# Performance work log

Measured on AMD Instinct MI355X. Metric: run time of the kernel, lower is better.

Reference implementation:

```python
import jax, jax.numpy as jnp
import numpy as np

N, E, B = 50000, 800000, 64
D_IN, D_E = 192, 64
NUM_OUT = 256


def setup_inputs() -> dict:
    key = jax.random.key(0)
    ks = jax.random.split(key, 30)
    rn = lambda k, s: jax.random.normal(k, s, dtype=jnp.float32) * 0.05
    return {
        "x": jax.random.normal(ks[0], (N, D_IN), jnp.float32),
        "edge_index": jax.random.randint(ks[1], (2, E), 0, N, dtype=jnp.int32),
        "edge_attr": jax.random.normal(ks[2], (E, D_E), jnp.float32),
        "batch": jnp.sort(jax.random.randint(ks[3], (N,), 0, B, dtype=jnp.int32)),
        "W1": rn(ks[4], (D_IN, 256)), "as1": rn(ks[5], (4, 64)), "ad1": rn(ks[6], (4, 64)),
        "We1": rn(ks[7], (D_E, 256)), "ae1": rn(ks[8], (4, 64)), "b1": rn(ks[9], (256,)),
        "W2": rn(ks[10], (256, 256)), "as2": rn(ks[11], (4, 64)), "ad2": rn(ks[12], (4, 64)),
        "We2": rn(ks[13], (D_E, 256)), "ae2": rn(ks[14], (4, 64)), "b2": rn(ks[15], (256,)),
        "W3": rn(ks[16], (256, 512)), "as3": rn(ks[17], (4, 128)), "ad3": rn(ks[18], (4, 128)),
        "We3": rn(ks[19], (D_E, 512)), "ae3": rn(ks[20], (4, 128)), "b3": rn(ks[21], (128,)),
        "Wa": rn(ks[22], (128, NUM_OUT)), "ba": rn(ks[23], (NUM_OUT,)),
        "Wv": rn(ks[24], (128, 1)), "bv": rn(ks[25], (1,)),
    }


def reference(x, edge_index, edge_attr, batch,
              W1, as1, ad1, We1, ae1, b1,
              W2, as2, ad2, We2, ae2, b2,
              W3, as3, ad3, We3, ae3, b3,
              Wa, ba, Wv, bv):
    Nn = x.shape[0]
    src0, dst0 = edge_index[0], edge_index[1]
    # PyG add_self_loops(fill_value='mean'): self-loop edge_attr = mean of incoming edge_attr
    deg = jax.ops.segment_sum(jnp.ones_like(dst0, dtype=x.dtype), dst0, num_segments=Nn)
    loop_attr = jax.ops.segment_sum(edge_attr, dst0, num_segments=Nn) / jnp.maximum(deg, 1.0)[:, None]
    loop = jnp.arange(Nn, dtype=src0.dtype)
    src = jnp.concatenate([src0, loop])
    dst = jnp.concatenate([dst0, loop])
    ea = jnp.concatenate([edge_attr, loop_attr], axis=0)

    def gat(h, W, a_s, a_d, We, a_e, bias, concat):
        Hh, C = a_s.shape
        hs = (h @ W).reshape(Nn, Hh, C)                       # [N,H,C]
        al_s = (hs * a_s).sum(-1)                             # [N,H]
        al_d = (hs * a_d).sum(-1)                             # [N,H]
        al_e = ((ea @ We).reshape(-1, Hh, C) * a_e).sum(-1)   # [E+N,H]
        alpha = jax.nn.leaky_relu(al_s[src] + al_d[dst] + al_e, 0.2)
        amax = jax.ops.segment_max(alpha, dst, num_segments=Nn)
        w = jnp.exp(alpha - amax[dst])
        denom = jax.ops.segment_sum(w, dst, num_segments=Nn)
        w = w / (denom[dst] + 1e-16)                          # scatter-softmax over dst
        out = jax.ops.segment_sum(hs[src] * w[..., None], dst, num_segments=Nn)
        out = out.reshape(Nn, Hh * C) if concat else out.mean(axis=1)
        return out + bias

    h = jax.nn.relu(gat(x, W1, as1, ad1, We1, ae1, b1, True))
    h = jax.nn.relu(gat(h, W2, as2, ad2, We2, ae2, b2, True))
    h = gat(h, W3, as3, ad3, We3, ae3, b3, False)
    cnt = jax.ops.segment_sum(jnp.ones((Nn,), h.dtype), batch, num_segments=B)
    g = jax.ops.segment_sum(h, batch, num_segments=B) / jnp.maximum(cnt, 1.0)[:, None]
    logits = g @ Wa + ba
    value = g @ Wv + bv
    return jnp.concatenate([logits, value], axis=-1)  # [B, num_outputs+1]
```

## Files before the change

### kernel.cpp

```cpp
#include <hip/hip_runtime.h>
#include <hip/hip_bf16.h>


typedef __attribute__((ext_vector_type(8))) short short8;
typedef __attribute__((ext_vector_type(4))) float floatx4;

#define DEV __device__ __forceinline__

DEV unsigned short f2b(float f) {
  union { float f; unsigned u; } v; v.f = f;
  unsigned r = v.u + 0x7FFFu + ((v.u >> 16) & 1u);
  return (unsigned short)(r >> 16);
}
DEV float b2f(unsigned short u) {
  union { unsigned u; float f; } v; v.u = ((unsigned)u) << 16;
  return v.f;
}

__global__ void k_deg(const int* __restrict__ dst, int* __restrict__ deg, int E) {
  int e = blockIdx.x * 256 + threadIdx.x;
  if (e < E) atomicAdd(&deg[dst[e]], 1);
}

__global__ __launch_bounds__(256) void k_scan1(const int* __restrict__ deg,
    int* __restrict__ rowptr, int* __restrict__ bsum, int N) {
  __shared__ int sd[256];
  int b = blockIdx.x, tid = threadIdx.x;
  int i0 = b * 1024 + tid * 4;
  int v[4]; int s = 0;
#pragma unroll
  for (int j = 0; j < 4; j++) { int i = i0 + j; v[j] = (i < N) ? deg[i] : 0; s += v[j]; }
  sd[tid] = s;
  __syncthreads();
  for (int off = 1; off < 256; off <<= 1) {
    int t = (tid >= off) ? sd[tid - off] : 0;
    __syncthreads();
    sd[tid] += t;
    __syncthreads();
  }
  int run = sd[tid] - s;
#pragma unroll
  for (int j = 0; j < 4; j++) { int i = i0 + j; if (i < N) rowptr[i] = run; run += v[j]; }
  if (tid == 255) bsum[b] = sd[255];
}

__global__ __launch_bounds__(256) void k_scan2(int* __restrict__ bsum, int nb) {
  __shared__ int sd[256];
  int tid = threadIdx.x;
  int v = (tid < nb) ? bsum[tid] : 0;
  sd[tid] = v;
  __syncthreads();
  for (int off = 1; off < 256; off <<= 1) {
    int t = (tid >= off) ? sd[tid - off] : 0;
    __syncthreads();
    sd[tid] += t;
    __syncthreads();
  }
  if (tid < nb) bsum[tid] = sd[tid] - v;
}

__global__ __launch_bounds__(256) void k_scan3(int* __restrict__ rowptr,
    int* __restrict__ cursor, const int* __restrict__ bsum, int N, int E) {
  int b = blockIdx.x, tid = threadIdx.x;
  int add = bsum[b];
  int i0 = b * 1024 + tid * 4;
#pragma unroll
  for (int j = 0; j < 4; j++) {
    int i = i0 + j;
    if (i < N) { int r = rowptr[i] + add; rowptr[i] = r; cursor[i] = r; }
  }
  if (b == 0 && tid == 0) rowptr[N] = E;
}

__global__ void k_scatter(const int* __restrict__ src, const int* __restrict__ dst,
    int* __restrict__ cursor, int2* __restrict__ csr, int E) {
  int e = blockIdx.x * 256 + threadIdx.x;
  if (e < E) {
    int d = dst[e];
    int pos = atomicAdd(&cursor[d], 1);
    csr[pos] = make_int2(src[e], e);
  }
}

__global__ void k_wt(const float* __restrict__ W, unsigned short* __restrict__ Wt,
                     int K, int Nout) {
  int idx = blockIdx.x * 256 + threadIdx.x;
  if (idx < K * Nout) {
    int n = idx / K, k = idx - n * K;
    Wt[idx] = f2b(W[(size_t)k * Nout + n]);
  }
}

__global__ void k_wep(const float* __restrict__ We1, const float* __restrict__ ae1,
                      const float* __restrict__ We2, const float* __restrict__ ae2,
                      const float* __restrict__ We3, const float* __restrict__ ae3,
                      unsigned short* __restrict__ Wept) {
  int t = blockIdx.x * 256 + threadIdx.x;
  int j = t >> 6, c = t & 63;
  int L = j >> 2, h = j & 3;
  const float* We = (L == 0) ? We1 : (L == 1) ? We2 : We3;
  const float* ae = (L == 0) ? ae1 : (L == 1) ? ae2 : ae3;
  int C = (L == 2) ? 128 : 64;
  int HC = 4 * C;
  float s = 0.f;
  for (int cc = 0; cc < C; cc++) s += We[(size_t)c * HC + h * C + cc] * ae[h * C + cc];
  Wept[j * 64 + c] = f2b(s);
  if (t < 256) {
    int jj = 12 + (t >> 6);
    Wept[jj * 64 + (t & 63)] = 0;
  }
}

template<bool A_F32, int OUT_MODE, bool DO_ALD>
__global__ __launch_bounds__(256) void k_gemm(const void* __restrict__ Ap,
    const unsigned short* __restrict__ Bt, void* __restrict__ Cp,
    int M, int Nout, int K, int EN,
    const float* __restrict__ a_s, const float* __restrict__ a_d,
    float* __restrict__ als, float* __restrict__ ald) {
  __shared__ unsigned short As[64][40];
  __shared__ unsigned short Bs[64][40];
  const int tid = threadIdx.x;
  const int wave = tid >> 6, lane = tid & 63;
  const int quad = lane >> 4, l16 = lane & 15;
  const int m0 = blockIdx.x * 64, n0 = blockIdx.y * 64;
  const int arow = tid >> 2, acg = (tid & 3) * 8;
  floatx4 acc[4] = {{0,0,0,0},{0,0,0,0},{0,0,0,0},{0,0,0,0}};
  for (int k0 = 0; k0 < K; k0 += 32) {
    {
      int gm = m0 + arow;
      unsigned short tmp[8];
      if (A_F32) {
        const float* Af = (const float*)Ap;
        if (gm < M) {
          const float4* p = (const float4*)(Af + (size_t)gm * K + k0 + acg);
          float4 u0 = p[0], u1 = p[1];
          tmp[0]=f2b(u0.x); tmp[1]=f2b(u0.y); tmp[2]=f2b(u0.z); tmp[3]=f2b(u0.w);
          tmp[4]=f2b(u1.x); tmp[5]=f2b(u1.y); tmp[6]=f2b(u1.z); tmp[7]=f2b(u1.w);
        } else {
#pragma unroll
          for (int j = 0; j < 8; j++) tmp[j] = 0;
        }
      } else {
        const unsigned short* Ab = (const unsigned short*)Ap;
        uint4 u = {0,0,0,0};
        if (gm < M) u = *(const uint4*)(Ab + (size_t)gm * K + k0 + acg);
        *(uint4*)tmp = u;
      }
      *(uint4*)&As[arow][acg] = *(uint4*)tmp;
      int gn = n0 + arow;
      uint4 bv = {0,0,0,0};
      if (gn < Nout) bv = *(const uint4*)(Bt + (size_t)gn * K + k0 + acg);
      *(uint4*)&Bs[arow][acg] = bv;
    }
    __syncthreads();
    short8 a = *(const short8*)&As[wave * 16 + l16][quad * 8];
#pragma unroll
    for (int t = 0; t < 4; t++) {
      short8 b = *(const short8*)&Bs[t * 16 + l16][quad * 8];
      acc[t] = __builtin_amdgcn_mfma_f32_16x16x32_bf16(a, b, acc[t], 0, 0, 0);
    }
    __syncthreads();
  }
#pragma unroll
  for (int t = 0; t < 4; t++) {
#pragma unroll
    for (int r = 0; r < 4; r++) {
      int row = m0 + wave * 16 + quad * 4 + r;
      int col = n0 + t * 16 + l16;
      float v = acc[t][r];
      if (OUT_MODE == 0) {
        if (row < M && col < Nout)
          ((unsigned short*)Cp)[(size_t)row * Nout + col] = f2b(v);
      } else {
        if (row < M && col < 12)
          ((float*)Cp)[((size_t)(col >> 2) * EN + row) * 4 + (col & 3)] = v;
      }
    }
  }
  if constexpr (DO_ALD) {
    int h = (n0 * 4) / Nout;
#pragma unroll
    for (int r = 0; r < 4; r++) {
      float ps = 0.f, pd = 0.f;
#pragma unroll
      for (int t = 0; t < 4; t++) {
        int col = n0 + t * 16 + l16;
        float v = acc[t][r];
        ps += v * a_s[col];
        pd += v * a_d[col];
      }
#pragma unroll
      for (int off = 1; off < 16; off <<= 1) {
        ps += __shfl_xor(ps, off, 64);
        pd += __shfl_xor(pd, off, 64);
      }
      int row = m0 + wave * 16 + quad * 4 + r;
      if (l16 == 0 && row < M) {
        atomicAdd(&als[row * 4 + h], ps);
        atomicAdd(&ald[row * 4 + h], pd);
      }
    }
  }
}

__global__ void k_loop_ale(const int* __restrict__ rowptr, const int2* __restrict__ csr,
                           float* __restrict__ ale, int N, int E) {
  int n = blockIdx.x * 256 + threadIdx.x;
  if (n >= N) return;
  const size_t EN = (size_t)E + N;
  int s = rowptr[n], e = rowptr[n + 1];
  float a[12];
#pragma unroll
  for (int j = 0; j < 12; j++) a[j] = 0.f;
  for (int p = s; p < e; p++) {
    int eid = csr[p].y;
#pragma unroll
    for (int L = 0; L < 3; L++) {
      float4 v = *(const float4*)(ale + (L * EN + eid) * 4);
      a[L * 4 + 0] += v.x; a[L * 4 + 1] += v.y;
      a[L * 4 + 2] += v.z; a[L * 4 + 3] += v.w;
    }
  }
  float inv = 1.0f / (float)((e - s) > 1 ? (e - s) : 1);
#pragma unroll
  for (int L = 0; L < 3; L++)
    *(float4*)(ale + (L * EN + E + n) * 4) =
        make_float4(a[L*4+0]*inv, a[L*4+1]*inv, a[L*4+2]*inv, a[L*4+3]*inv);
}

template<int VPL, int MODE>
__global__ __launch_bounds__(256) void k_gath(const unsigned short* __restrict__ hs,
    const int* __restrict__ rowptr, const int2* __restrict__ csr,
    const float* __restrict__ ale,
    const float* __restrict__ als, const float* __restrict__ ald,
    const float* __restrict__ bias, unsigned short* __restrict__ outb,
    float* __restrict__ outf, int N, int E) {
  constexpr int U = (VPL == 16) ? 8 : 4;
  constexpr int NV = VPL / 8;
  const int HC = 16 * VPL;
  const int lane = threadIdx.x & 63;
  const int grp = lane >> 4, sl = lane & 15, hd = sl >> 2;
  const int node = blockIdx.x * 16 + (threadIdx.x >> 6) * 4 + grp;
  if (node >= N) return;
  const int start = rowptr[node];
  const int cnt = rowptr[node + 1] - start;
  const float aldh = ald[node * 4 + hd];
  float acc[VPL];
#pragma unroll
  for (int j = 0; j < VPL; j++) acc[j] = 0.f;
  float den = 0.f;
  for (int base = 0; base < cnt; base += U) {
    int sp[U]; float pw[U];
#pragma unroll
    for (int e = 0; e < U; e++) {
      int idx = base + e;
      int idc = idx < cnt ? idx : cnt - 1;
      int2 se = csr[start + idc];
      sp[e] = se.x;
      float av = als[(size_t)se.x * 4 + hd] + aldh + ale[(size_t)se.y * 4 + hd];
      av = av > 0.f ? av : 0.2f * av;
      float p = __expf(av);
      pw[e] = idx < cnt ? p : 0.f;
    }
    uint4 dv[U][NV];
#pragma unroll
    for (int e = 0; e < U; e++) {
      const uint4* rp = (const uint4*)(hs + (size_t)sp[e] * HC + sl * VPL);
#pragma unroll
      for (int q = 0; q < NV; q++) dv[e][q] = rp[q];
    }
#pragma unroll
    for (int e = 0; e < U; e++) {
      den += pw[e];
      const unsigned short* vs = (const unsigned short*)&dv[e][0];
#pragma unroll
      for (int j = 0; j < VPL; j++) acc[j] += pw[e] * b2f(vs[j]);
    }
  }
  {
    float av = als[(size_t)node * 4 + hd] + aldh + ale[((size_t)E + node) * 4 + hd];
    av = av > 0.f ? av : 0.2f * av;
    float p = __expf(av);
    den += p;
    const uint4* rp = (const uint4*)(hs + (size_t)node * HC + sl * VPL);
#pragma unroll
    for (int q = 0; q < NV; q++) {
      uint4 u = rp[q];
      const unsigned short* vs = (const unsigned short*)&u;
#pragma unroll
      for (int j = 0; j < 8; j++) acc[q * 8 + j] += p * b2f(vs[j]);
    }
  }
  float inv = 1.0f / (den + 1e-16f);
  if constexpr (MODE == 0) {
    unsigned short tmp[VPL];
#pragma unroll
    for (int j = 0; j < VPL; j++) {
      float v = acc[j] * inv + bias[sl * VPL + j];
      tmp[j] = f2b(fmaxf(v, 0.f));
    }
    unsigned short* op = outb + (size_t)node * HC + sl * VPL;
#pragma unroll
    for (int q = 0; q < NV; q++) ((uint4*)op)[q] = ((uint4*)tmp)[q];
  } else {
#pragma unroll
    for (int j = 0; j < VPL; j++) {
      float v = acc[j] * inv;
      v += __shfl_xor(v, 4, 64);
      v += __shfl_xor(v, 8, 64);
      acc[j] = v * 0.25f;
    }
    if (sl < 4) {
      float* op = outf + (size_t)node * (4 * VPL) + sl * VPL;
#pragma unroll
      for (int j = 0; j < VPL; j++) op[j] = acc[j] + bias[sl * VPL + j];
    }
  }
}

__global__ __launch_bounds__(256) void k_pool(const float* __restrict__ out3,
    const int* __restrict__ bat, float* __restrict__ g, int* __restrict__ cntb, int N) {
  int wid = blockIdx.x * 4 + (threadIdx.x >> 6);
  int lane = threadIdx.x & 63;
  int per = (N + 255) / 256;
  int s = wid * per, e = s + per;
  if (e > N) e = N;
  if (s >= e) return;
  int cur = bat[s];
  float ax = 0.f, ay = 0.f; int run = 0;
  for (int n = s; n < e; n++) {
    int b = bat[n];
    if (b != cur) {
      atomicAdd(&g[cur * 128 + lane * 2], ax);
      atomicAdd(&g[cur * 128 + lane * 2 + 1], ay);
      if (lane == 0) atomicAdd(&cntb[cur], run);
      ax = 0.f; ay = 0.f; run = 0; cur = b;
    }
    float2 v = *(const float2*)(out3 + (size_t)n * 128 + lane * 2);
    ax += v.x; ay += v.y; run++;
  }
  atomicAdd(&g[cur * 128 + lane * 2], ax);
  atomicAdd(&g[cur * 128 + lane * 2 + 1], ay);
  if (lane == 0) atomicAdd(&cntb[cur], run);
}

__global__ __launch_bounds__(320) void k_final(const float* __restrict__ g,
    const int* __restrict__ cntb, const float* __restrict__ Wa, const float* __restrict__ ba,
    const float* __restrict__ Wv, const float* __restrict__ bv, float* __restrict__ out) {
  __shared__ float gm[128];
  int b = blockIdx.x, t = threadIdx.x;
  if (t < 128) {
    float c = (float)cntb[b];
    gm[t] = g[b * 128 + t] / fmaxf(c, 1.f);
  }
  __syncthreads();
  if (t < 257) {
    float acc = 0.f;
    if (t < 256) {
      for (int k = 0; k < 128; k++) acc += gm[k] * Wa[k * 256 + t];
      acc += ba[t];
    } else {
      for (int k = 0; k < 128; k++) acc += gm[k] * Wv[k];
      acc += bv[0];
    }
    out[b * 257 + t] = acc;
  }
}

extern "C" void kernel_launch(void* const* d_in, const int* in_sizes, int n_in,
                              void* d_out, int out_size, void* d_ws, size_t ws_size,
                              hipStream_t stream) {
  const float* x   = (const float*)d_in[0];
  const int*   ei  = (const int*)  d_in[1];
  const float* ea  = (const float*)d_in[2];
  const int*   bat = (const int*)  d_in[3];
  const float* W1  = (const float*)d_in[4];
  const float* as1 = (const float*)d_in[5];
  const float* ad1 = (const float*)d_in[6];
  const float* We1 = (const float*)d_in[7];
  const float* ae1 = (const float*)d_in[8];
  const float* b1  = (const float*)d_in[9];
  const float* W2  = (const float*)d_in[10];
  const float* as2 = (const float*)d_in[11];
  const float* ad2 = (const float*)d_in[12];
  const float* We2 = (const float*)d_in[13];
  const float* ae2 = (const float*)d_in[14];
  const float* b2  = (const float*)d_in[15];
  const float* W3  = (const float*)d_in[16];
  const float* as3 = (const float*)d_in[17];
  const float* ad3 = (const float*)d_in[18];
  const float* We3 = (const float*)d_in[19];
  const float* ae3 = (const float*)d_in[20];
  const float* b3  = (const float*)d_in[21];
  const float* Wa  = (const float*)d_in[22];
  const float* ba  = (const float*)d_in[23];
  const float* Wv  = (const float*)d_in[24];
  const float* bv  = (const float*)d_in[25];
  (void)n_in; (void)out_size; (void)ws_size;

  const int N = in_sizes[0] / 192;
  const int E = in_sizes[1] / 2;
  const size_t EN = (size_t)E + N;
  const int* srcv = ei;
  const int* dstv = ei + E;
  const int nb = (N + 1023) / 1024;

  size_t off = 0;
  auto alloc = [&](size_t bytes) -> char* {
    char* p = (char*)d_ws + off;
    off += (bytes + 255) & ~(size_t)255;
    return p;
  };
  int* deg     = (int*)alloc((size_t)N * 4);
  int* rowptr  = (int*)alloc((size_t)(N + 1) * 4);
  int* cursor  = (int*)alloc((size_t)N * 4);
  int* bsum    = (int*)alloc(256 * 4);
  int2* csr    = (int2*)alloc((size_t)E * 8);
  float* ale   = (float*)alloc(3 * EN * 4 * 4);
  unsigned short* Wept = (unsigned short*)alloc(16 * 64 * 2);
  unsigned short* W1t  = (unsigned short*)alloc(256 * 192 * 2);
  unsigned short* W2t  = (unsigned short*)alloc(256 * 256 * 2);
  unsigned short* W3t  = (unsigned short*)alloc(512 * 256 * 2);
  unsigned short* hs   = (unsigned short*)alloc((size_t)N * 512 * 2);
  unsigned short* h1   = (unsigned short*)alloc((size_t)N * 256 * 2);
  unsigned short* h2   = (unsigned short*)alloc((size_t)N * 256 * 2);
  float* out3  = (float*)alloc((size_t)N * 128 * 4);
  float* als_all = (float*)alloc((size_t)N * 4 * 4 * 6);
  float* g     = (float*)alloc(64 * 128 * 4 + 64 * 4);
  int* cntb    = (int*)(g + 64 * 128);
  float* als1 = als_all + (size_t)N * 4 * 0;
  float* ald1 = als_all + (size_t)N * 4 * 1;
  float* als2 = als_all + (size_t)N * 4 * 2;
  float* ald2 = als_all + (size_t)N * 4 * 3;
  float* als3 = als_all + (size_t)N * 4 * 4;
  float* ald3 = als_all + (size_t)N * 4 * 5;

  hipMemsetAsync(deg, 0, (size_t)N * 4, stream);
  hipMemsetAsync(als_all, 0, (size_t)N * 4 * 4 * 6, stream);
  hipMemsetAsync(g, 0, 64 * 128 * 4 + 64 * 4, stream);

  k_deg<<<(E + 255) / 256, 256, 0, stream>>>(dstv, deg, E);
  k_scan1<<<nb, 256, 0, stream>>>(deg, rowptr, bsum, N);
  k_scan2<<<1, 256, 0, stream>>>(bsum, nb);
  k_scan3<<<nb, 256, 0, stream>>>(rowptr, cursor, bsum, N, E);
  k_scatter<<<(E + 255) / 256, 256, 0, stream>>>(srcv, dstv, cursor, csr, E);
  k_wt<<<(192 * 256 + 255) / 256, 256, 0, stream>>>(W1, W1t, 192, 256);
  k_wt<<<(256 * 256 + 255) / 256, 256, 0, stream>>>(W2, W2t, 256, 256);
  k_wt<<<(256 * 512 + 255) / 256, 256, 0, stream>>>(W3, W3t, 256, 512);
  k_wep<<<3, 256, 0, stream>>>(We1, ae1, We2, ae2, We3, ae3, Wept);
  k_gemm<true, 2, false><<<dim3((E + 63) / 64, 1), 256, 0, stream>>>(
      ea, Wept, ale, E, 16, 64, (int)EN, nullptr, nullptr, nullptr, nullptr);
  k_loop_ale<<<(N + 255) / 256, 256, 0, stream>>>(rowptr, csr, ale, N, E);
  k_gemm<true, 0, true><<<dim3((N + 63) / 64, 4), 256, 0, stream>>>(
      x, W1t, hs, N, 256, 192, 0, as1, ad1, als1, ald1);
  k_gath<16, 0><<<(N + 15) / 16, 256, 0, stream>>>(
      hs, rowptr, csr, ale + 0 * EN * 4, als1, ald1, b1, h1, nullptr, N, E);
  k_gemm<false, 0, true><<<dim3((N + 63) / 64, 4), 256, 0, stream>>>(
      h1, W2t, hs, N, 256, 256, 0, as2, ad2, als2, ald2);
  k_gath<16, 0><<<(N + 15) / 16, 256, 0, stream>>>(
      hs, rowptr, csr, ale + 1 * EN * 4, als2, ald2, b2, h2, nullptr, N, E);
  k_gemm<false, 0, true><<<dim3((N + 63) / 64, 8), 256, 0, stream>>>(
      h2, W3t, hs, N, 512, 256, 0, as3, ad3, als3, ald3);
  k_gath<32, 1><<<(N + 15) / 16, 256, 0, stream>>>(
      hs, rowptr, csr, ale + 2 * EN * 4, als3, ald3, b3, nullptr, out3, N, E);
  k_pool<<<64, 256, 0, stream>>>(out3, bat, g, cntb, N);
  k_final<<<64, 320, 0, stream>>>(g, cntb, Wa, ba, Wv, bv, (float*)d_out);
}
```

Before: 1.148 ms.

## Interleave per-layer edge logits in one row layout and use 8 lanes per node in gathers

The edge-attention logits for all three layers now sit in one row of 16 floats per edge instead of three separate planes. The GEMM writes each row contiguously, and the self-loop mean kernel uses four threads per node, each reading float4 chunks. The layer-1/2 gather kernels now assign 8 lanes per node with 32 values each (32 nodes per block) rather than 16 lanes with 16 values, and the unroll factor drops from 8 to 4. The aim is better locality for ale reads and more nodes in flight per block. The cost is a higher per-lane register load and a 64-byte row stride for each 4-byte logit read in the gathers.

```diff
diff --git a/kernel.cpp b/kernel.cpp
--- a/kernel.cpp
+++ b/kernel.cpp
@@ -114,7 +114,7 @@
 template<bool A_F32, int OUT_MODE, bool DO_ALD>
 __global__ __launch_bounds__(256) void k_gemm(const void* __restrict__ Ap,
     const unsigned short* __restrict__ Bt, void* __restrict__ Cp,
-    int M, int Nout, int K, int EN,
+    int M, int Nout, int K,
     const float* __restrict__ a_s, const float* __restrict__ a_d,
     float* __restrict__ als, float* __restrict__ ald) {
   __shared__ unsigned short As[64][40];
@@ -173,7 +173,7 @@
           ((unsigned short*)Cp)[(size_t)row * Nout + col] = f2b(v);
       } else {
         if (row < M && col < 12)
-          ((float*)Cp)[((size_t)(col >> 2) * EN + row) * 4 + (col & 3)] = v;
+          ((float*)Cp)[(size_t)row * 16 + col] = v;
       }
     }
   }
@@ -203,44 +203,44 @@
   }
 }
 
-__global__ void k_loop_ale(const int* __restrict__ rowptr, const int2* __restrict__ csr,
-                           float* __restrict__ ale, int N, int E) {
-  int n = blockIdx.x * 256 + threadIdx.x;
-  if (n >= N) return;
-  const size_t EN = (size_t)E + N;
-  int s = rowptr[n], e = rowptr[n + 1];
-  float a[12];
-#pragma unroll
-  for (int j = 0; j < 12; j++) a[j] = 0.f;
-  for (int p = s; p < e; p++) {
-    int eid = csr[p].y;
-#pragma unroll
-    for (int L = 0; L < 3; L++) {
-      float4 v = *(const float4*)(ale + (L * EN + eid) * 4);
-      a[L * 4 + 0] += v.x; a[L * 4 + 1] += v.y;
-      a[L * 4 + 2] += v.z; a[L * 4 + 3] += v.w;
+__global__ __launch_bounds__(256) void k_loop_ale(const int* __restrict__ rowptr,
+    const int2* __restrict__ csr, float* __restrict__ ale, int N, int E) {
+  int t = blockIdx.x * 256 + threadIdx.x;
+  int node = t >> 2, q = t & 3;
+  if (node >= N) return;
+  int s = rowptr[node], e = rowptr[node + 1];
+  float4 a = make_float4(0.f, 0.f, 0.f, 0.f);
+  if (q < 3) {
+    for (int p = s; p < e; p++) {
+      int eid = csr[p].y;
+      float4 v = *(const float4*)(ale + (size_t)eid * 16 + q * 4);
+      a.x += v.x; a.y += v.y; a.z += v.z; a.w += v.w;
     }
   }
   float inv = 1.0f / (float)((e - s) > 1 ? (e - s) : 1);
-#pragma unroll
-  for (int L = 0; L < 3; L++)
-    *(float4*)(ale + (L * EN + E + n) * 4) =
-        make_float4(a[L*4+0]*inv, a[L*4+1]*inv, a[L*4+2]*inv, a[L*4+3]*inv);
-}
-
-template<int VPL, int MODE>
+  if (q < 3)
+    *(float4*)(ale + ((size_t)E + node) * 16 + q * 4) =
+        make_float4(a.x * inv, a.y * inv, a.z * inv, a.w * inv);
+}
+
+template<int LPN, int VPL, int MODE>
 __global__ __launch_bounds__(256) void k_gath(const unsigned short* __restrict__ hs,
     const int* __restrict__ rowptr, const int2* __restrict__ csr,
     const float* __restrict__ ale,
+    int L4,
     const float* __restrict__ als, const float* __restrict__ ald,
     const float* __restrict__ bias, unsigned short* __restrict__ outb,
     float* __restrict__ outf, int N, int E) {
-  constexpr int U = (VPL == 16) ? 8 : 4;
+  constexpr int U = 4;
   constexpr int NV = VPL / 8;
-  const int HC = 16 * VPL;
+  constexpr int HC = LPN * VPL;
+  constexpr int SH = (LPN == 8) ? 1 : 2;
+  constexpr int NPB = 256 / LPN;
   const int lane = threadIdx.x & 63;
-  const int grp = lane >> 4, sl = lane & 15, hd = sl >> 2;
-  const int node = blockIdx.x * 16 + (threadIdx.x >> 6) * 4 + grp;
+  const int sl = lane & (LPN - 1);
+  const int grp = lane / LPN;
+  const int hd = sl >> SH;
+  const int node = blockIdx.x * NPB + (threadIdx.x >> 6) * (64 / LPN) + grp;
   if (node >= N) return;
   const int start = rowptr[node];
   const int cnt = rowptr[node + 1] - start;
@@ -257,7 +257,8 @@
       int idc = idx < cnt ? idx : cnt - 1;
       int2 se = csr[start + idc];
       sp[e] = se.x;
-      float av = als[(size_t)se.x * 4 + hd] + aldh + ale[(size_t)se.y * 4 + hd];
+      float av = als[(size_t)se.x * 4 + hd] + aldh +
+                 ale[(size_t)se.y * 16 + L4 + hd];
       av = av > 0.f ? av : 0.2f * av;
       float p = __expf(av);
       pw[e] = idx < cnt ? p : 0.f;
@@ -278,7 +279,8 @@
     }
   }
   {
-    float av = als[(size_t)node * 4 + hd] + aldh + ale[((size_t)E + node) * 4 + hd];
+    float av = als[(size_t)node * 4 + hd] + aldh +
+               ale[((size_t)E + node) * 16 + L4 + hd];
     av = av > 0.f ? av : 0.2f * av;
     float p = __expf(av);
     den += p;
@@ -416,7 +418,7 @@
   int* cursor  = (int*)alloc((size_t)N * 4);
   int* bsum    = (int*)alloc(256 * 4);
   int2* csr    = (int2*)alloc((size_t)E * 8);
-  float* ale   = (float*)alloc(3 * EN * 4 * 4);
+  float* ale   = (float*)alloc(EN * 16 * 4);
   unsigned short* Wept = (unsigned short*)alloc(16 * 64 * 2);
   unsigned short* W1t  = (unsigned short*)alloc(256 * 192 * 2);
   unsigned short* W2t  = (unsigned short*)alloc(256 * 256 * 2);
@@ -449,20 +451,20 @@
   k_wt<<<(256 * 512 + 255) / 256, 256, 0, stream>>>(W3, W3t, 256, 512);
   k_wep<<<3, 256, 0, stream>>>(We1, ae1, We2, ae2, We3, ae3, Wept);
   k_gemm<true, 2, false><<<dim3((E + 63) / 64, 1), 256, 0, stream>>>(
-      ea, Wept, ale, E, 16, 64, (int)EN, nullptr, nullptr, nullptr, nullptr);
-  k_loop_ale<<<(N + 255) / 256, 256, 0, stream>>>(rowptr, csr, ale, N, E);
+      ea, Wept, ale, E, 16, 64, nullptr, nullptr, nullptr, nullptr);
+  k_loop_ale<<<(N * 4 + 255) / 256, 256, 0, stream>>>(rowptr, csr, ale, N, E);
   k_gemm<true, 0, true><<<dim3((N + 63) / 64, 4), 256, 0, stream>>>(
-      x, W1t, hs, N, 256, 192, 0, as1, ad1, als1, ald1);
-  k_gath<16, 0><<<(N + 15) / 16, 256, 0, stream>>>(
-      hs, rowptr, csr, ale + 0 * EN * 4, als1, ald1, b1, h1, nullptr, N, E);
+      x, W1t, hs, N, 256, 192, as1, ad1, als1, ald1);
+  k_gath<8, 32, 0><<<(N + 31) / 32, 256, 0, stream>>>(
+      hs, rowptr, csr, ale, 0, als1, ald1, b1, h1, nullptr, N, E);
   k_gemm<false, 0, true><<<dim3((N + 63) / 64, 4), 256, 0, stream>>>(
-      h1, W2t, hs, N, 256, 256, 0, as2, ad2, als2, ald2);
-  k_gath<16, 0><<<(N + 15) / 16, 256, 0, stream>>>(
-      hs, rowptr, csr, ale + 1 * EN * 4, als2, ald2, b2, h2, nullptr, N, E);
+      h1, W2t, hs, N, 256, 256, as2, ad2, als2, ald2);
+  k_gath<8, 32, 0><<<(N + 31) / 32, 256, 0, stream>>>(
+      hs, rowptr, csr, ale, 4, als2, ald2, b2, h2, nullptr, N, E);
   k_gemm<false, 0, true><<<dim3((N + 63) / 64, 8), 256, 0, stream>>>(
-      h2, W3t, hs, N, 512, 256, 0, as3, ad3, als3, ald3);
-  k_gath<32, 1><<<(N + 15) / 16, 256, 0, stream>>>(
-      hs, rowptr, csr, ale + 2 * EN * 4, als3, ald3, b3, nullptr, out3, N, E);
+      h2, W3t, hs, N, 512, 256, as3, ad3, als3, ald3);
+  k_gath<16, 32, 1><<<(N + 15) / 16, 256, 0, stream>>>(
+      hs, rowptr, csr, ale, 8, als3, ald3, b3, nullptr, out3, N, E);
   k_pool<<<64, 256, 0, stream>>>(out3, bat, g, cntb, N);
   k_final<<<64, 320, 0, stream>>>(g, cntb, Wa, ba, Wv, bv, (float*)d_out);
 }
```

Result: faster. 1.067 ms (-7.0%).
